# Kernel optimization log

Hardware: AMD Instinct MI355X
Metric: run time of the kernel (lower is better)

The kernel has to match this reference:

```python
import jax, jax.numpy as jnp
import numpy as np

PAD = (1, 2, 1, 1, 0, 1)  # (W_left, W_right, H_top, H_bottom, D_front, D_back)
K = 3  # pool kernel
S = 2  # pool stride


def setup_inputs() -> dict:
    key = jax.random.key(0)
    x = jax.random.normal(key, (8, 32, 16, 64, 256), dtype=jnp.float32)
    return {"x": x}


def reference(x):
    pl, pr, pt, pb, pf, pk = PAD
    # ZeroPad3d: pads last three dims (D, H, W)
    x_p = jnp.pad(x, ((0, 0), (0, 0), (pf, pk), (pt, pb), (pl, pr)))
    N, C, Dp, Hp, Wp = x_p.shape
    Cp = C * Dp * Hp
    x_seq = x_p.reshape(N, Cp, Wp)

    # MaxPool1d with indices along W
    L = (Wp - K) // S + 1
    starts = jnp.arange(L) * S                      # [L]
    win_idx = starts[:, None] + jnp.arange(K)       # [L, K]
    windows = x_seq[..., win_idx]                   # [N, Cp, L, K]
    off = jnp.argmax(windows, axis=-1)              # [N, Cp, L]
    idx = starts[None, None, :] + off               # global indices into W
    pooled = jnp.take_along_axis(x_seq, idx, axis=-1)  # [N, Cp, L]

    # Softsign
    act = pooled / (1.0 + jnp.abs(pooled))

    # MaxUnpool1d: scatter activated values back at argmax positions.
    # Duplicate indices (overlapping windows) carry identical values, so
    # scatter-set order is irrelevant.
    n_ix = jnp.arange(N)[:, None, None]
    c_ix = jnp.arange(Cp)[None, :, None]
    unpooled = jnp.zeros_like(x_seq).at[n_ix, c_ix, idx].set(act)  # [N, Cp, Wp]

    fused = unpooled.reshape(N, C, Dp, Hp, Wp) + x_p
    return fused.mean(axis=2)  # [N, C, Hp, Wp]
```

## Files before the change

kernel.cpp:

```cpp
#include <hip/hip_runtime.h>


#define NN 8
#define CC 32
#define DD 16
#define HH 64
#define WW 256
#define HP 66
#define WP 259

__global__ __launch_bounds__(256) void fused_pool_kernel(const float* __restrict__ x,
                                                         float* __restrict__ out) {
    const int wid  = blockIdx.x * 4 + (threadIdx.x >> 6);
    const int lane = threadIdx.x & 63;
    const int hp   = wid % HP;
    const int nc   = wid / HP;

    float* orow = out + (size_t)wid * WP;
    const int w0 = 4 * lane + 1;

    if (hp == 0 || hp == HP - 1) {
        orow[w0] = 0.f; orow[w0 + 1] = 0.f; orow[w0 + 2] = 0.f; orow[w0 + 3] = 0.f;
        if (lane == 0) { orow[0] = 0.f; orow[WW + 1] = 0.f; orow[WW + 2] = 0.f; }
        return;
    }
    const int h = hp - 1;
    const float* xbase = x + (((size_t)nc * DD * HH) + h) * WW + 4 * lane;

    float4 b[DD];
#pragma unroll
    for (int d = 0; d < DD; ++d)
        b[d] = *reinterpret_cast<const float4*>(xbase + (size_t)d * HH * WW);

    float a0 = 0.f, a1 = 0.f, a2 = 0.f, a3 = 0.f;
#pragma unroll
    for (int d = 0; d < DD; ++d) {
        const float b0 = b[d].x, b1 = b[d].y, b2 = b[d].z, b3 = b[d].w;
        float pm1 = __shfl_up(b3, 1, 64);
        float np0 = __shfl_down(b0, 1, 64);
        float np1 = __shfl_down(b1, 1, 64);
        if (lane == 0)  pm1 = 0.f;
        if (lane == 63) { np0 = 0.f; np1 = 0.f; }

        const bool h0 = (b0 > pm1) & (b0 >= b1);
        const bool h1 = ((b1 >= b2) & (b1 >= b3)) | ((b1 > pm1) & (b1 > b0));
        const bool h2 = (b2 > b1) & (b2 >= b3);
        const bool h3 = ((b3 >= np0) & (b3 >= np1)) | ((b3 > b1) & (b3 > b2));

        a0 += b0 + (h0 ? b0 * __builtin_amdgcn_rcpf(1.f + fabsf(b0)) : 0.f);
        a1 += b1 + (h1 ? b1 * __builtin_amdgcn_rcpf(1.f + fabsf(b1)) : 0.f);
        a2 += b2 + (h2 ? b2 * __builtin_amdgcn_rcpf(1.f + fabsf(b2)) : 0.f);
        a3 += b3 + (h3 ? b3 * __builtin_amdgcn_rcpf(1.f + fabsf(b3)) : 0.f);
    }

    const float inv = 1.0f / 17.0f;
    orow[w0]     = a0 * inv;
    orow[w0 + 1] = a1 * inv;
    orow[w0 + 2] = a2 * inv;
    orow[w0 + 3] = a3 * inv;
    if (lane == 0) { orow[0] = 0.f; orow[WW + 1] = 0.f; orow[WW + 2] = 0.f; }
}

extern "C" void kernel_launch(void* const* d_in, const int* in_sizes, int n_in,
                              void* d_out, int out_size, void* d_ws, size_t ws_size,
                              hipStream_t stream) {
    const float* x = (const float*)d_in[0];
    float* out = (float*)d_out;
    const int rows = NN * CC * HP;
    fused_pool_kernel<<<rows / 4, 256, 0, stream>>>(x, out);
}
```

Baseline: 47.59 us.

## Process four rows per wave with double-buffered loads and vectorized stores

Each wave now handles four output rows instead of one. Loads for the next row are issued in two halves while the current row is computed, so memory latency overlaps with compute. Pad rows are handled by a zero scale factor instead of an early return. Output is written as an aligned float4 by shifting a3 across lanes. The pad rows still load real data, which wastes some bandwidth, and the grid gets four times fewer waves, which lowers parallelism.

```diff
diff --git a/kernel.cpp b/kernel.cpp
--- a/kernel.cpp
+++ b/kernel.cpp
@@ -8,57 +8,78 @@
 #define WW 256
 #define HP 66
 #define WP 259
+#define ROWS (NN * CC * HP)
+#define RPW 4
+#define NWAVES (ROWS / RPW)
+#define SLICE (HH * WW)
 
-__global__ __launch_bounds__(256) void fused_pool_kernel(const float* __restrict__ x,
-                                                         float* __restrict__ out) {
-    const int wid  = blockIdx.x * 4 + (threadIdx.x >> 6);
+typedef float4 f4;
+
+__global__ __launch_bounds__(256, 4) void fused_pool_kernel(const float* __restrict__ x,
+                                                            float* __restrict__ out) {
+    const int wv   = blockIdx.x * 4 + (threadIdx.x >> 6);
     const int lane = threadIdx.x & 63;
-    const int hp   = wid % HP;
-    const int nc   = wid / HP;
+    const bool l0 = (lane == 0), l63 = (lane == 63);
 
-    float* orow = out + (size_t)wid * WP;
-    const int w0 = 4 * lane + 1;
-
-    if (hp == 0 || hp == HP - 1) {
-        orow[w0] = 0.f; orow[w0 + 1] = 0.f; orow[w0 + 2] = 0.f; orow[w0 + 3] = 0.f;
-        if (lane == 0) { orow[0] = 0.f; orow[WW + 1] = 0.f; orow[WW + 2] = 0.f; }
-        return;
-    }
-    const int h = hp - 1;
-    const float* xbase = x + (((size_t)nc * DD * HH) + h) * WW + 4 * lane;
-
-    float4 b[DD];
+    const float* xb[RPW];
+    float*       ob[RPW];
+    float        sc[RPW];
 #pragma unroll
-    for (int d = 0; d < DD; ++d)
-        b[d] = *reinterpret_cast<const float4*>(xbase + (size_t)d * HH * WW);
-
-    float a0 = 0.f, a1 = 0.f, a2 = 0.f, a3 = 0.f;
-#pragma unroll
-    for (int d = 0; d < DD; ++d) {
-        const float b0 = b[d].x, b1 = b[d].y, b2 = b[d].z, b3 = b[d].w;
-        float pm1 = __shfl_up(b3, 1, 64);
-        float np0 = __shfl_down(b0, 1, 64);
-        float np1 = __shfl_down(b1, 1, 64);
-        if (lane == 0)  pm1 = 0.f;
-        if (lane == 63) { np0 = 0.f; np1 = 0.f; }
-
-        const bool h0 = (b0 > pm1) & (b0 >= b1);
-        const bool h1 = ((b1 >= b2) & (b1 >= b3)) | ((b1 > pm1) & (b1 > b0));
-        const bool h2 = (b2 > b1) & (b2 >= b3);
-        const bool h3 = ((b3 >= np0) & (b3 >= np1)) | ((b3 > b1) & (b3 > b2));
-
-        a0 += b0 + (h0 ? b0 * __builtin_amdgcn_rcpf(1.f + fabsf(b0)) : 0.f);
-        a1 += b1 + (h1 ? b1 * __builtin_amdgcn_rcpf(1.f + fabsf(b1)) : 0.f);
-        a2 += b2 + (h2 ? b2 * __builtin_amdgcn_rcpf(1.f + fabsf(b2)) : 0.f);
-        a3 += b3 + (h3 ? b3 * __builtin_amdgcn_rcpf(1.f + fabsf(b3)) : 0.f);
+    for (int i = 0; i < RPW; ++i) {
+        const int row = wv * RPW + i;
+        const int hp  = row % HP;
+        const int nc  = row / HP;
+        int h = hp - 1; h = h < 0 ? 0 : (h > HH - 1 ? HH - 1 : h);
+        xb[i] = x + (size_t)nc * DD * SLICE + (size_t)h * WW + 4 * lane;
+        ob[i] = out + (size_t)row * WP;
+        sc[i] = (hp == 0 || hp == HP - 1) ? 0.f : (1.0f / 17.0f);
     }
 
-    const float inv = 1.0f / 17.0f;
-    orow[w0]     = a0 * inv;
-    orow[w0 + 1] = a1 * inv;
-    orow[w0 + 2] = a2 * inv;
-    orow[w0 + 3] = a3 * inv;
-    if (lane == 0) { orow[0] = 0.f; orow[WW + 1] = 0.f; orow[WW + 2] = 0.f; }
+    f4 A0, A1, A2, A3, A4, A5, A6, A7, B0, B1, B2, B3, B4, B5, B6, B7;
+
+#define LD(base, d) (*reinterpret_cast<const f4*>((base) + (size_t)(d) * SLICE))
+#define LOADA(base) do { A0 = LD(base, 0); A1 = LD(base, 1); A2 = LD(base, 2); A3 = LD(base, 3); \
+                         A4 = LD(base, 4); A5 = LD(base, 5); A6 = LD(base, 6); A7 = LD(base, 7); } while (0)
+#define LOADB(base) do { B0 = LD(base, 8);  B1 = LD(base, 9);  B2 = LD(base, 10); B3 = LD(base, 11); \
+                         B4 = LD(base, 12); B5 = LD(base, 13); B6 = LD(base, 14); B7 = LD(base, 15); } while (0)
+
+#define SL(bb) do { \
+    const float b0 = (bb).x, b1 = (bb).y, b2 = (bb).z, b3 = (bb).w; \
+    float pm1 = __shfl_up(b3, 1, 64);   if (l0)  pm1 = 0.f; \
+    float np0 = __shfl_down(b0, 1, 64); \
+    float np1 = __shfl_down(b1, 1, 64); if (l63) { np0 = 0.f; np1 = 0.f; } \
+    const bool h0 = (b0 > pm1) & (b0 >= b1); \
+    const bool h1 = ((b1 >= b2) & (b1 >= b3)) | ((b1 > pm1) & (b1 > b0)); \
+    const bool h2 = (b2 > b1) & (b2 >= b3); \
+    const bool h3 = ((b3 >= np0) & (b3 >= np1)) | ((b3 > b1) & (b3 > b2)); \
+    a0 += b0 + (h0 ? b0 * __builtin_amdgcn_rcpf(1.f + fabsf(b0)) : 0.f); \
+    a1 += b1 + (h1 ? b1 * __builtin_amdgcn_rcpf(1.f + fabsf(b1)) : 0.f); \
+    a2 += b2 + (h2 ? b2 * __builtin_amdgcn_rcpf(1.f + fabsf(b2)) : 0.f); \
+    a3 += b3 + (h3 ? b3 * __builtin_amdgcn_rcpf(1.f + fabsf(b3)) : 0.f); \
+} while (0)
+
+    LOADA(xb[0]);
+    LOADB(xb[0]);
+
+#pragma unroll
+    for (int i = 0; i < RPW; ++i) {
+        float a0 = 0.f, a1 = 0.f, a2 = 0.f, a3 = 0.f;
+
+        SL(A0); SL(A1); SL(A2); SL(A3); SL(A4); SL(A5); SL(A6); SL(A7);
+        if (i + 1 < RPW) LOADA(xb[i + 1]);
+        SL(B0); SL(B1); SL(B2); SL(B3); SL(B4); SL(B5); SL(B6); SL(B7);
+        if (i + 1 < RPW) LOADB(xb[i + 1]);
+
+        float sa3 = __shfl_up(a3, 1, 64); if (l0) sa3 = 0.f;
+        const float s = sc[i];
+        f4 v; v.x = sa3 * s; v.y = a0 * s; v.z = a1 * s; v.w = a2 * s;
+        *reinterpret_cast<f4*>(ob[i] + 4 * lane) = v;
+        if (l63) { ob[i][256] = a3 * s; ob[i][257] = 0.f; ob[i][258] = 0.f; }
+    }
+#undef LD
+#undef LOADA
+#undef LOADB
+#undef SL
 }
 
 extern "C" void kernel_launch(void* const* d_in, const int* in_sizes, int n_in,
@@ -66,6 +87,5 @@
                               hipStream_t stream) {
     const float* x = (const float*)d_in[0];
     float* out = (float*)d_out;
-    const int rows = NN * CC * HP;
-    fused_pool_kernel<<<rows / 4, 256, 0, stream>>>(x, out);
+    fused_pool_kernel<<<NWAVES / 4, 256, 0, stream>>>(x, out);
 }
```

Result: slower. 55.01 us (+15.6%).
